# Kernel tuning notes

Measured on AMD Instinct MI355X. Metric: run time of the kernel, lower is better.

The kernel has to match this reference:

```python
import jax, jax.numpy as jnp
import numpy as np

B = 16      # number of point clouds
N = 4096    # points per cloud (max after densify)
D = 3       # xyz


def setup_inputs() -> dict:
    key = jax.random.key(0)
    k1, k2 = jax.random.split(key)
    pred = jax.random.normal(k1, (B * N, D), dtype=jnp.float32)
    target = jax.random.normal(k2, (B * N, D), dtype=jnp.float32)
    # sorted segment ids, equal-sized clouds (faithful to to_dense_batch usage)
    batch = jnp.repeat(jnp.arange(B, dtype=jnp.int64), N)
    return {"pred": pred, "target": target, "batch": batch}


def to_dense_batch(x, batch, num_batches, max_n):
    # PyG to_dense_batch: scatter flat points into [B, max_n, D], zero-padded.
    ones = jnp.ones_like(batch)
    counts = jax.ops.segment_sum(ones, batch, num_segments=num_batches)
    offsets = jnp.concatenate([jnp.zeros((1,), batch.dtype), jnp.cumsum(counts)[:-1]])
    pos = jnp.arange(batch.shape[0], dtype=batch.dtype) - offsets[batch]
    dense = jnp.zeros((num_batches, max_n, x.shape[-1]), x.dtype)
    return dense.at[batch, pos].set(x)


def chamfer_distance(x, y):
    # squared-euclidean pairwise distances via the GEMM identity
    x2 = jnp.sum(x * x, axis=-1)                      # [B, N]
    y2 = jnp.sum(y * y, axis=-1)                      # [B, M]
    xy = jnp.einsum('bnd,bmd->bnm', x, y)             # [B, N, M]
    d = x2[:, :, None] + y2[:, None, :] - 2.0 * xy    # [B, N, M]
    cham_x = jnp.mean(jnp.min(d, axis=2), axis=1)     # mean over N of min over M
    cham_y = jnp.mean(jnp.min(d, axis=1), axis=1)     # mean over M of min over N
    # point_reduction='mean', batch_reduction='mean' (pytorch3d defaults)
    return jnp.mean(cham_x + cham_y)


def reference(pred, target, batch):
    x = to_dense_batch(pred, batch, B, N)
    y = to_dense_batch(target, batch, B, N)
    return chamfer_distance(x, y)
```

## Files before the change

kernel.cpp:

```cpp
#include <hip/hip_runtime.h>


namespace {

constexpr int kB = 16;
constexpr int kN = 4096;
constexpr int kPlane = kB * kN;
constexpr int kJS = 4;
constexpr int kJSL = kN / kJS;
constexpr float kScale = 1.0f / (float)(kB * kN);

typedef short bf16x8 __attribute__((ext_vector_type(8)));
typedef float f32x16 __attribute__((ext_vector_type(16)));
typedef unsigned short u16;

__device__ inline u16 bf16_rn(float f) {
  union { float f; unsigned u; } v; v.f = f;
  unsigned r = v.u + 0x7fffu + ((v.u >> 16) & 1u);
  return (u16)(r >> 16);
}
__device__ inline float bf16_f(u16 h) {
  union { unsigned u; float f; } v; v.u = (unsigned)h << 16;
  return v.f;
}
__device__ inline unsigned pk2(u16 lo, u16 hi) {
  return (unsigned)lo | ((unsigned)hi << 16);
}

__global__ void init_out(float* out) { out[0] = 0.0f; }

__global__ __launch_bounds__(256) void cd_prep(
    const float* __restrict__ pred, const float* __restrict__ targ,
    u16* __restrict__ Ab, u16* __restrict__ Bb, float* __restrict__ out) {
  const int p = blockIdx.x * 256 + threadIdx.x;
  if (p == 0) out[0] = 0.0f;
  const u16 one = 0x3F80;
  {
    const float a = pred[3 * p], c = pred[3 * p + 1], d = pred[3 * p + 2];
    const u16 ah = bf16_rn(a), ch = bf16_rn(c), dh = bf16_rn(d);
    const u16 al = bf16_rn(a - bf16_f(ah));
    const u16 cl = bf16_rn(c - bf16_f(ch));
    const u16 dl = bf16_rn(d - bf16_f(dh));
    const float s2 = fmaf(a, a, fmaf(c, c, d * d));
    const u16 s2h = bf16_rn(s2);
    const u16 s2l = bf16_rn(s2 - bf16_f(s2h));
    uint4 w0, w1;
    w0.x = pk2(ah, ch); w0.y = pk2(dh, al); w0.z = pk2(cl, dl); w0.w = pk2(ah, ch);
    w1.x = pk2(dh, s2h); w1.y = pk2(s2l, one); w1.z = pk2(one, al); w1.w = pk2(cl, dl);
    uint4* dst = reinterpret_cast<uint4*>(Ab + (size_t)p * 16);
    dst[0] = w0; dst[1] = w1;
  }
  {
    const float a = targ[3 * p], c = targ[3 * p + 1], d = targ[3 * p + 2];
    const u16 ah0 = bf16_rn(a), ch0 = bf16_rn(c), dh0 = bf16_rn(d);
    const u16 ah = bf16_rn(-2.0f * bf16_f(ah0));
    const u16 ch = bf16_rn(-2.0f * bf16_f(ch0));
    const u16 dh = bf16_rn(-2.0f * bf16_f(dh0));
    const u16 al = bf16_rn(-2.0f * bf16_f(bf16_rn(a - bf16_f(ah0))));
    const u16 cl = bf16_rn(-2.0f * bf16_f(bf16_rn(c - bf16_f(ch0))));
    const u16 dl = bf16_rn(-2.0f * bf16_f(bf16_rn(d - bf16_f(dh0))));
    const float s2 = fmaf(a, a, fmaf(c, c, d * d));
    const u16 s2h = bf16_rn(s2);
    const u16 s2l = bf16_rn(s2 - bf16_f(s2h));
    uint4 w0, w1;
    w0.x = pk2(ah, ch); w0.y = pk2(dh, ah); w0.z = pk2(ch, dh); w0.w = pk2(al, cl);
    w1.x = pk2(dl, one); w1.y = pk2(one, s2h); w1.z = pk2(s2l, al); w1.w = pk2(cl, dl);
    uint4* dst = reinterpret_cast<uint4*>(Bb + (size_t)p * 16);
    dst[0] = w0; dst[1] = w1;
  }
}

__global__ __launch_bounds__(256) void cd_mfma(
    const u16* __restrict__ Ab, const u16* __restrict__ Bb,
    float* __restrict__ colpart, float* __restrict__ rowpart) {
  __shared__ float clds[4 * kJSL];

  const int t = threadIdx.x;
  const int w = t >> 6, lane = t & 63;
  const int half = lane >> 5, l31 = lane & 31;
  const int chunk = blockIdx.x;
  const int cloud = blockIdx.y;
  const int slice = blockIdx.z;

  const int arow = cloud * kN + chunk * 128 + w * 32 + l31;
  const bf16x8 afrag = *(const bf16x8*)(Ab + (size_t)arow * 16 + half * 8);

  f32x16 zacc;
#pragma unroll
  for (int r = 0; r < 16; ++r) zacc[r] = 0.0f;
  float rmin[16];
#pragma unroll
  for (int r = 0; r < 16; ++r) rmin[r] = 1e30f;

  const u16* bbase = Bb + ((size_t)cloud * kN + slice * kJSL) * 16;
  constexpr int NT = kJSL / 64;
  const int jcol = l31 * 16 + half * 8;
  bf16x8 b0 = *(const bf16x8*)(bbase + jcol);
  bf16x8 b1 = *(const bf16x8*)(bbase + 32 * 16 + jcol);
  for (int jt = 0; jt < NT; ++jt) {
    const int nx = ((jt + 1) & (NT - 1)) * 64 * 16;
    const bf16x8 n0 = *(const bf16x8*)(bbase + nx + jcol);
    const bf16x8 n1 = *(const bf16x8*)(bbase + nx + 32 * 16 + jcol);
    const f32x16 s0 = __builtin_amdgcn_mfma_f32_32x32x16_bf16(afrag, b0, zacc, 0, 0, 0);
    const f32x16 s1 = __builtin_amdgcn_mfma_f32_32x32x16_bf16(afrag, b1, zacc, 0, 0, 0);
    float cm0 = s0[0], cm1 = s1[0];
#pragma unroll
    for (int r = 1; r < 16; ++r) { cm0 = fminf(cm0, s0[r]); cm1 = fminf(cm1, s1[r]); }
#pragma unroll
    for (int r = 0; r < 16; ++r) rmin[r] = fminf(rmin[r], fminf(s0[r], s1[r]));
    cm0 = fminf(cm0, __shfl_xor(cm0, 32, 64));
    cm1 = fminf(cm1, __shfl_xor(cm1, 32, 64));
    if (half == 0) {
      clds[w * kJSL + jt * 64 + l31] = cm0;
      clds[w * kJSL + jt * 64 + 32 + l31] = cm1;
    }
    b0 = n0; b1 = n1;
  }

#pragma unroll
  for (int st = 1; st < 32; st <<= 1) {
#pragma unroll
    for (int r = 0; r < 16; ++r)
      rmin[r] = fminf(rmin[r], __shfl_xor(rmin[r], st, 64));
  }
  if (l31 == 0) {
    float* rp = rowpart + ((size_t)slice * kB + cloud) * kN + chunk * 128 + w * 32;
#pragma unroll
    for (int r = 0; r < 16; ++r) {
      const int row = (r & 3) + 8 * (r >> 2) + 4 * half;
      rp[row] = rmin[r];
    }
  }

  __syncthreads();
  for (int j = t; j < kJSL; j += 256) {
    const float m = fminf(fminf(clds[j], clds[kJSL + j]),
                          fminf(clds[2 * kJSL + j], clds[3 * kJSL + j]));
    colpart[((size_t)cloud * 32 + chunk) * kN + slice * kJSL + j] = m;
  }
}

__global__ __launch_bounds__(256) void cd_reduce(
    const float* __restrict__ colpart, const float* __restrict__ rowpart,
    float* __restrict__ out) {
  const int u = blockIdx.x * 256 + threadIdx.x;
  const int cloud = u >> 12, p = u & (kN - 1);
  float rm = 1e30f;
#pragma unroll
  for (int s2 = 0; s2 < kJS; ++s2)
    rm = fminf(rm, rowpart[((size_t)s2 * kB + cloud) * kN + p]);
  const float* cp = colpart + (size_t)cloud * 32 * kN + p;
  float cm = 1e30f;
#pragma unroll 8
  for (int c = 0; c < 32; ++c) cm = fminf(cm, cp[(size_t)c * kN]);
  float s = rm + cm;
  for (int o = 32; o > 0; o >>= 1) s += __shfl_down(s, o, 64);
  __shared__ float wsum[4];
  const int lane = threadIdx.x & 63, wv = threadIdx.x >> 6;
  if (lane == 0) wsum[wv] = s;
  __syncthreads();
  if (threadIdx.x == 0)
    atomicAdd(out, (wsum[0] + wsum[1] + wsum[2] + wsum[3]) * kScale);
}

template <int KX>
__global__ __launch_bounds__(256) void chamfer_direct(
    const float* __restrict__ pred, const float* __restrict__ targ,
    float* __restrict__ out) {
  __shared__ float4 tA[128], tB[128];
  const int t = threadIdx.x;
  const int xb = blockIdx.x, b = blockIdx.y, dir = blockIdx.z;
  const float* __restrict__ X = dir ? targ : pred;
  const float* __restrict__ Y = dir ? pred : targ;
  float2 xx2[KX], xy2[KX], xz2[KX];
  float x2[KX], mn[KX];
  const int ibase = b * kN + xb * (256 * KX) + t;
#pragma unroll
  for (int k = 0; k < KX; ++k) {
    const int i = ibase + k * 256;
    const float a = X[3 * i], c = X[3 * i + 1], d = X[3 * i + 2];
    x2[k] = fmaf(a, a, fmaf(c, c, d * d));
    xx2[k] = make_float2(-2.0f * a, -2.0f * a);
    xy2[k] = make_float2(-2.0f * c, -2.0f * c);
    xz2[k] = make_float2(-2.0f * d, -2.0f * d);
    mn[k] = 1e30f;
  }
  for (int t0 = 0; t0 < kN; t0 += 256) {
    __syncthreads();
    if (t < 128) {
      const int j0 = 3 * (b * kN + t0 + 2 * t);
      const float a0 = Y[j0], c0 = Y[j0 + 1], d0 = Y[j0 + 2];
      const float a1 = Y[j0 + 3], c1 = Y[j0 + 4], d1 = Y[j0 + 5];
      tA[t] = make_float4(a0, a1, c0, c1);
      tB[t] = make_float4(d0, d1, fmaf(a0, a0, fmaf(c0, c0, d0 * d0)),
                          fmaf(a1, a1, fmaf(c1, c1, d1 * d1)));
    }
    __syncthreads();
    for (int jj = 0; jj < 128; ++jj) {
      const float4 qa = tA[jj], qb = tB[jj];
      const float2 qx = make_float2(qa.x, qa.y), qy = make_float2(qa.z, qa.w);
      const float2 qz = make_float2(qb.x, qb.y), qw = make_float2(qb.z, qb.w);
#pragma unroll
      for (int k = 0; k < KX; ++k) {
        float2 acc;
        asm("v_pk_fma_f32 %0, %1, %2, %3\n\t"
            "v_pk_fma_f32 %0, %4, %5, %0\n\t"
            "v_pk_fma_f32 %0, %6, %7, %0"
            : "=&v"(acc)
            : "v"(xz2[k]), "v"(qz), "v"(qw), "v"(xy2[k]), "v"(qy),
              "v"(xx2[k]), "v"(qx));
        asm("v_min3_f32 %0, %0, %1, %2" : "+v"(mn[k]) : "v"(acc.x), "v"(acc.y));
      }
    }
  }
  float s = 0.0f;
#pragma unroll
  for (int k = 0; k < KX; ++k) s += x2[k] + mn[k];
  for (int o = 32; o > 0; o >>= 1) s += __shfl_down(s, o, 64);
  __shared__ float wsum[4];
  const int lane = t & 63, wv = t >> 6;
  if (lane == 0) wsum[wv] = s;
  __syncthreads();
  if (t == 0)
    atomicAdd(out, (wsum[0] + wsum[1] + wsum[2] + wsum[3]) * kScale);
}

}

extern "C" void kernel_launch(void* const* d_in, const int* in_sizes, int n_in,
                              void* d_out, int out_size, void* d_ws,
                              size_t ws_size, hipStream_t stream) {
  const float* pred = (const float*)d_in[0];
  const float* targ = (const float*)d_in[1];
  float* out = (float*)d_out;

  const size_t needA = (size_t)kPlane * 16 * sizeof(u16);
  const size_t needCol = (size_t)kB * 32 * kN * sizeof(float);
  const size_t needRow = (size_t)kJS * kPlane * sizeof(float);
  if (ws_size >= 2 * needA + needCol + needRow) {
    u16* Ab = (u16*)d_ws;
    u16* Bb = (u16*)((char*)d_ws + needA);
    float* colpart = (float*)((char*)d_ws + 2 * needA);
    float* rowpart = (float*)((char*)d_ws + 2 * needA + needCol);
    cd_prep<<<dim3(kPlane / 256), 256, 0, stream>>>(pred, targ, Ab, Bb, out);
    cd_mfma<<<dim3(32, kB, kJS), 256, 0, stream>>>(Ab, Bb, colpart, rowpart);
    cd_reduce<<<dim3(kPlane / 256), 256, 0, stream>>>(colpart, rowpart, out);
  } else {
    init_out<<<dim3(1), dim3(1), 0, stream>>>(out);
    constexpr int KX = 8;
    dim3 grid(kN / (256 * KX), kB, 2);
    chamfer_direct<KX><<<grid, 256, 0, stream>>>(pred, targ, out);
  }
}
```

Baseline: 96.05 us.

## Compute both chamfer directions as row-min passes instead of column-min via LDS

Replaces the single MFMA pass that tracked both row minima and column minima (column minima through LDS and a large colpart buffer) with two symmetric row-min passes, one per direction, with A and B operands swapped. This doubles the MFMA work but drops the per-tile column reduction, the cross-half shuffles, the LDS stores and the 32-way colpart reduction. It also changes the slice count from 4 to 2 and drops the explicit register prefetch of B fragments in favour of unroll 2. The reduce kernel now sums row minima over both directions.

```diff
diff --git a/kernel.cpp b/kernel.cpp
--- a/kernel.cpp
+++ b/kernel.cpp
@@ -6,7 +6,7 @@
 constexpr int kB = 16;
 constexpr int kN = 4096;
 constexpr int kPlane = kB * kN;
-constexpr int kJS = 4;
+constexpr int kJS = 2;
 constexpr int kJSL = kN / kJS;
 constexpr float kScale = 1.0f / (float)(kB * kN);
 
@@ -70,20 +70,23 @@
   }
 }
 
-__global__ __launch_bounds__(256) void cd_mfma(
+__global__ __launch_bounds__(256) void cd_rowmin(
     const u16* __restrict__ Ab, const u16* __restrict__ Bb,
-    float* __restrict__ colpart, float* __restrict__ rowpart) {
-  __shared__ float clds[4 * kJSL];
-
+    float* __restrict__ rowpart) {
   const int t = threadIdx.x;
   const int w = t >> 6, lane = t & 63;
   const int half = lane >> 5, l31 = lane & 31;
   const int chunk = blockIdx.x;
   const int cloud = blockIdx.y;
-  const int slice = blockIdx.z;
+  const int z = blockIdx.z;
+  const int dir = z / kJS;
+  const int slice = z % kJS;
+
+  const u16* __restrict__ RowM = dir ? Bb : Ab;
+  const u16* __restrict__ ColM = dir ? Ab : Bb;
 
   const int arow = cloud * kN + chunk * 128 + w * 32 + l31;
-  const bf16x8 afrag = *(const bf16x8*)(Ab + (size_t)arow * 16 + half * 8);
+  const bf16x8 afrag = *(const bf16x8*)(RowM + (size_t)arow * 16 + half * 8);
 
   f32x16 zacc;
 #pragma unroll
@@ -92,29 +95,19 @@
 #pragma unroll
   for (int r = 0; r < 16; ++r) rmin[r] = 1e30f;
 
-  const u16* bbase = Bb + ((size_t)cloud * kN + slice * kJSL) * 16;
+  const u16* bbase = ColM + ((size_t)cloud * kN + slice * kJSL) * 16;
   constexpr int NT = kJSL / 64;
   const int jcol = l31 * 16 + half * 8;
-  bf16x8 b0 = *(const bf16x8*)(bbase + jcol);
-  bf16x8 b1 = *(const bf16x8*)(bbase + 32 * 16 + jcol);
+#pragma unroll 2
   for (int jt = 0; jt < NT; ++jt) {
-    const int nx = ((jt + 1) & (NT - 1)) * 64 * 16;
-    const bf16x8 n0 = *(const bf16x8*)(bbase + nx + jcol);
-    const bf16x8 n1 = *(const bf16x8*)(bbase + nx + 32 * 16 + jcol);
+    const u16* bp = bbase + jt * 64 * 16;
+    const bf16x8 b0 = *(const bf16x8*)(bp + jcol);
+    const bf16x8 b1 = *(const bf16x8*)(bp + 32 * 16 + jcol);
     const f32x16 s0 = __builtin_amdgcn_mfma_f32_32x32x16_bf16(afrag, b0, zacc, 0, 0, 0);
     const f32x16 s1 = __builtin_amdgcn_mfma_f32_32x32x16_bf16(afrag, b1, zacc, 0, 0, 0);
-    float cm0 = s0[0], cm1 = s1[0];
-#pragma unroll
-    for (int r = 1; r < 16; ++r) { cm0 = fminf(cm0, s0[r]); cm1 = fminf(cm1, s1[r]); }
-#pragma unroll
-    for (int r = 0; r < 16; ++r) rmin[r] = fminf(rmin[r], fminf(s0[r], s1[r]));
-    cm0 = fminf(cm0, __shfl_xor(cm0, 32, 64));
-    cm1 = fminf(cm1, __shfl_xor(cm1, 32, 64));
-    if (half == 0) {
-      clds[w * kJSL + jt * 64 + l31] = cm0;
-      clds[w * kJSL + jt * 64 + 32 + l31] = cm1;
-    }
-    b0 = n0; b1 = n1;
+#pragma unroll
+    for (int r = 0; r < 16; ++r)
+      rmin[r] = fminf(rmin[r], fminf(s0[r], s1[r]));
   }
 
 #pragma unroll
@@ -124,36 +117,25 @@
       rmin[r] = fminf(rmin[r], __shfl_xor(rmin[r], st, 64));
   }
   if (l31 == 0) {
-    float* rp = rowpart + ((size_t)slice * kB + cloud) * kN + chunk * 128 + w * 32;
+    float* rp = rowpart + ((size_t)z * kB + cloud) * kN + chunk * 128 + w * 32;
 #pragma unroll
     for (int r = 0; r < 16; ++r) {
       const int row = (r & 3) + 8 * (r >> 2) + 4 * half;
       rp[row] = rmin[r];
     }
   }
-
-  __syncthreads();
-  for (int j = t; j < kJSL; j += 256) {
-    const float m = fminf(fminf(clds[j], clds[kJSL + j]),
-                          fminf(clds[2 * kJSL + j], clds[3 * kJSL + j]));
-    colpart[((size_t)cloud * 32 + chunk) * kN + slice * kJSL + j] = m;
-  }
 }
 
 __global__ __launch_bounds__(256) void cd_reduce(
-    const float* __restrict__ colpart, const float* __restrict__ rowpart,
-    float* __restrict__ out) {
+    const float* __restrict__ rowpart, float* __restrict__ out) {
   const int u = blockIdx.x * 256 + threadIdx.x;
-  const int cloud = u >> 12, p = u & (kN - 1);
+  const int dir = u >> 16, rest = u & (kPlane - 1);
+  const int cloud = rest >> 12, p = rest & (kN - 1);
   float rm = 1e30f;
 #pragma unroll
   for (int s2 = 0; s2 < kJS; ++s2)
-    rm = fminf(rm, rowpart[((size_t)s2 * kB + cloud) * kN + p]);
-  const float* cp = colpart + (size_t)cloud * 32 * kN + p;
-  float cm = 1e30f;
-#pragma unroll 8
-  for (int c = 0; c < 32; ++c) cm = fminf(cm, cp[(size_t)c * kN]);
-  float s = rm + cm;
+    rm = fminf(rm, rowpart[(((size_t)(dir * kJS + s2)) * kB + cloud) * kN + p]);
+  float s = rm;
   for (int o = 32; o > 0; o >>= 1) s += __shfl_down(s, o, 64);
   __shared__ float wsum[4];
   const int lane = threadIdx.x & 63, wv = threadIdx.x >> 6;
@@ -235,16 +217,14 @@
   float* out = (float*)d_out;
 
   const size_t needA = (size_t)kPlane * 16 * sizeof(u16);
-  const size_t needCol = (size_t)kB * 32 * kN * sizeof(float);
-  const size_t needRow = (size_t)kJS * kPlane * sizeof(float);
-  if (ws_size >= 2 * needA + needCol + needRow) {
+  const size_t needRow = (size_t)2 * kJS * kPlane * sizeof(float);
+  if (ws_size >= 2 * needA + needRow) {
     u16* Ab = (u16*)d_ws;
     u16* Bb = (u16*)((char*)d_ws + needA);
-    float* colpart = (float*)((char*)d_ws + 2 * needA);
-    float* rowpart = (float*)((char*)d_ws + 2 * needA + needCol);
+    float* rowpart = (float*)((char*)d_ws + 2 * needA);
     cd_prep<<<dim3(kPlane / 256), 256, 0, stream>>>(pred, targ, Ab, Bb, out);
-    cd_mfma<<<dim3(32, kB, kJS), 256, 0, stream>>>(Ab, Bb, colpart, rowpart);
-    cd_reduce<<<dim3(kPlane / 256), 256, 0, stream>>>(colpart, rowpart, out);
+    cd_rowmin<<<dim3(32, kB, 2 * kJS), 256, 0, stream>>>(Ab, Bb, rowpart);
+    cd_reduce<<<dim3(2 * kPlane / 256), 256, 0, stream>>>(rowpart, out);
   } else {
     init_out<<<dim3(1), dim3(1), 0, stream>>>(out);
     constexpr int KX = 8;
```

After: 114.1 us. 1.19x slower.
